# Kernel optimization log

Measured on AMD Instinct MI355X. Metric: run time of the kernel, lower is better.

The kernel has to match this reference:

```python
import jax, jax.numpy as jnp
import numpy as np

PI = np.pi


def setup_inputs() -> dict:
    key = jax.random.key(0)
    ks = jax.random.split(key, 20)
    B, L, D = 2, 1024, 512
    TP = 16      # n_sets(4) * planes_per_set(4)
    PP = 16      # pos_planes
    MAXL = 8192
    sc = 1.0 / np.sqrt(D)
    return {
        "x": jax.random.normal(ks[0], (B, L, D), jnp.float32),
        "Wk": jax.random.normal(ks[1], (TP, D), jnp.float32) * sc,
        "bk": jnp.zeros((TP,), jnp.float32),
        "Wq": jax.random.normal(ks[2], (TP, D), jnp.float32) * sc,
        "bq": jnp.zeros((TP,), jnp.float32),
        "Wv": jax.random.normal(ks[3], (D, D), jnp.float32) * sc,
        "bv": jnp.zeros((D,), jnp.float32),
        "ln_g": jnp.ones((D,), jnp.float32),
        "ln_b": jnp.zeros((D,), jnp.float32),
        "Wo": jax.random.normal(ks[4], (D, D), jnp.float32) * sc,
        "bo": jnp.zeros((D,), jnp.float32),
        "set_w": jnp.ones((4,), jnp.float32),
        "pos_phases": jax.random.normal(ks[5], (MAXL, PP), jnp.float32) * PI,
        "pos_weight": jnp.ones((1,), jnp.float32),
        "Wg1": jax.random.normal(ks[6], (D // 2, D), jnp.float32) * sc,
        "bg1": jnp.zeros((D // 2,), jnp.float32),
        "Wg2": jax.random.normal(ks[7], (1, D // 2), jnp.float32) * np.sqrt(2.0 / D),
        "bg2": jnp.zeros((1,), jnp.float32),
    }


def reference(x, Wk, bk, Wq, bq, Wv, bv, ln_g, ln_b, Wo, bo,
              set_w, pos_phases, pos_weight, Wg1, bg1, Wg2, bg2):
    B, L, D = x.shape
    n_sets, pps = 4, 4

    # --- content phasor memory ---
    kp = jnp.tanh(x @ Wk.T + bk) * PI                       # [B,L,16]
    qp = jnp.tanh(x @ Wq.T + bq) * PI
    key_ph = jnp.exp(1j * kp).reshape(B, L, n_sets, pps)    # [B,L,S,P] c64
    qry_ph = jnp.exp(1j * qp).reshape(B, L, n_sets, pps)
    Vr = x @ Wv.T + bv                                       # [B,L,D]
    V = Vr.astype(jnp.complex64)

    bound = key_ph[..., None] * V[:, :, None, None, :]       # [B,L,S,P,D] c64
    mem = jnp.cumsum(bound, axis=1)                          # prefix-sum memory
    retr = (mem * jnp.conj(qry_ph)[..., None]).sum(axis=3).real   # [B,L,S,D]
    w = jax.nn.softmax(set_w)
    content = (retr * w[None, None, :, None]).sum(axis=2)    # [B,L,D]

    # --- positional cos/sin memory ---
    ph = pos_phases[:L]                                      # [L,PP]
    c = jnp.cos(ph)[None]                                    # [1,L,PP]
    s = jnp.sin(ph)[None]
    br = Vr[:, :, None, :] * c[..., None]                    # [B,L,PP,D]
    bi = Vr[:, :, None, :] * s[..., None]
    mr = jnp.cumsum(br, axis=1)
    mi = jnp.cumsum(bi, axis=1)
    pos = (mr * c[..., None] + mi * s[..., None]).sum(axis=2)  # [B,L,D]

    # --- gate, mix, normalize, output proj ---
    g = jax.nn.sigmoid(
        jax.nn.gelu(x @ Wg1.T + bg1, approximate=False) @ Wg2.T + bg2)  # [B,L,1]
    total = g * content + (1.0 - g) * jax.nn.sigmoid(pos_weight) * pos
    norm = jnp.sqrt(jnp.arange(1, L + 1, dtype=x.dtype) * pps)[None, :, None]
    t = total / norm
    mu = t.mean(-1, keepdims=True)
    var = ((t - mu) ** 2).mean(-1, keepdims=True)
    tn = (t - mu) / jnp.sqrt(var + 1e-5) * ln_g + ln_b
    return x + tn @ Wo.T + bo
```

## Files before the change

kernel.cpp:

```cpp
#include <hip/hip_runtime.h>
#include <math.h>

#define PI_F 3.14159265358979323846f
#define BB 2
#define LL 1024
#define DD 512
#define NCH 64
#define CHUNK 32
#define NCHUNK (LL/CHUNK)
#define YN 896
#define NW 1408

typedef __attribute__((ext_vector_type(8))) short short8;
typedef __attribute__((ext_vector_type(4))) float floatx4;
typedef const __attribute__((address_space(1))) unsigned int cgu32;
typedef __attribute__((address_space(3))) unsigned int lu32;

__device__ __forceinline__ unsigned short f2bf(float f){
    unsigned u = __float_as_uint(f);
    unsigned r = (u + 0x7fff + ((u >> 16) & 1)) >> 16;
    return (unsigned short)r;
}

__global__ __launch_bounds__(128) void k_prep(
    const float* __restrict__ Wv, const float* __restrict__ Wg1,
    const float* __restrict__ Wk, const float* __restrict__ Wq,
    const float* __restrict__ Wo,
    const float* __restrict__ bv, const float* __restrict__ bg1,
    const float* __restrict__ bk, const float* __restrict__ bq,
    const float* __restrict__ bo,
    unsigned short* __restrict__ Wb, float* __restrict__ bcat)
{
    const int n = blockIdx.x, tid = threadIdx.x;
    const float* src = (n<512) ? Wv  + (size_t)n*512
                     : (n<768) ? Wg1 + (size_t)(n-512)*512
                     : (n<784) ? Wk  + (size_t)(n-768)*512
                     : (n<800) ? Wq  + (size_t)(n-784)*512
                     : (n<896) ? (const float*)0
                               : Wo  + (size_t)(n-896)*512;
    float4 v = make_float4(0.f,0.f,0.f,0.f);
    if (src) v = ((const float4*)src)[tid];
    ushort4 o; o.x=f2bf(v.x); o.y=f2bf(v.y); o.z=f2bf(v.z); o.w=f2bf(v.w);
    ((ushort4*)(Wb + (size_t)n*512))[tid] = o;
    if (tid == 0)
        bcat[n] = (n<512)?bv[n] : (n<768)?bg1[n-512] : (n<784)?bk[n-768]
                : (n<800)?bq[n-784] : (n<896)?0.f : bo[n-896];
}

__global__ __launch_bounds__(256) void k_xb(
    const float* __restrict__ x, unsigned short* __restrict__ xb)
{
    const int i = blockIdx.x*256 + threadIdx.x;
    float4 v = ((const float4*)x)[i];
    ushort4 o; o.x=f2bf(v.x); o.y=f2bf(v.y); o.z=f2bf(v.z); o.w=f2bf(v.w);
    ((ushort4*)xb)[i] = o;
}

__device__ __forceinline__ void gemm64x64(
    const unsigned short* Ag, const unsigned short* Bg,
    short* As, short* Bs, int tid, floatx4 acc[2][2])
{
    const int lane = tid & 63, w = tid >> 6;
    const int wm = w & 1, wn = w >> 1;
    const int q = lane >> 4, m15 = lane & 15;
    for (int kt = 0; kt < 512; kt += 64) {
        __syncthreads();
        #pragma unroll
        for (int i = 0; i < 2; ++i) {
            const int rowbase = (w*2 + i) * 8;
            const int r  = rowbase + (lane >> 3);
            const int gb = (lane & 7) ^ (r & 7);
            const unsigned short* ga = Ag + (size_t)r*512 + kt + gb*8;
            const unsigned short* gbp = Bg + (size_t)r*512 + kt + gb*8;
            __builtin_amdgcn_global_load_lds((cgu32*)(const void*)ga,
                                             (lu32*)(As + rowbase*64), 16, 0, 0);
            __builtin_amdgcn_global_load_lds((cgu32*)(const void*)gbp,
                                             (lu32*)(Bs + rowbase*64), 16, 0, 0);
        }
        __syncthreads();
        #pragma unroll
        for (int k32 = 0; k32 < 64; k32 += 32) {
            short8 af[2], bf[2];
            #pragma unroll
            for (int t = 0; t < 2; ++t) {
                const int ra  = 32*wm + 16*t + m15;
                const int sba = ((k32>>3) + q) ^ (ra & 7);
                af[t] = *(const short8*)(As + ra*64 + sba*8);
                const int rb  = 32*wn + 16*t + m15;
                const int sbb = ((k32>>3) + q) ^ (rb & 7);
                bf[t] = *(const short8*)(Bs + rb*64 + sbb*8);
            }
            #pragma unroll
            for (int mt = 0; mt < 2; ++mt)
                #pragma unroll
                for (int nt = 0; nt < 2; ++nt)
                    acc[mt][nt] = __builtin_amdgcn_mfma_f32_16x16x32_bf16(
                        af[mt], bf[nt], acc[mt][nt], 0, 0, 0);
        }
    }
}

__global__ __launch_bounds__(256) void kg1(
    const unsigned short* __restrict__ xb, const unsigned short* __restrict__ Wb,
    const float* __restrict__ bcat, float* __restrict__ Y)
{
    __shared__ short As[64*64], Bs[64*64];
    const int tid = threadIdx.x;
    const int row0 = blockIdx.x*64, n0 = blockIdx.y*64;
    floatx4 acc[2][2];
    #pragma unroll
    for (int mt=0;mt<2;++mt)
        #pragma unroll
        for (int nt=0;nt<2;++nt) acc[mt][nt] = (floatx4){0.f,0.f,0.f,0.f};
    gemm64x64(xb + (size_t)row0*512, Wb + (size_t)n0*512, As, Bs, tid, acc);
    const int lane = tid & 63, w = tid >> 6;
    const int wm = w & 1, wn = w >> 1, q = lane >> 4, m15 = lane & 15;
    #pragma unroll
    for (int mt=0;mt<2;++mt)
        #pragma unroll
        for (int nt=0;nt<2;++nt){
            const int n = n0 + 32*wn + 16*nt + m15;
            const float b = bcat[n];
            #pragma unroll
            for (int reg=0;reg<4;++reg){
                const int m = row0 + 32*wm + 16*mt + q*4 + reg;
                Y[(size_t)m*YN + n] = acc[mt][nt][reg] + b;
            }
        }
}

__global__ __launch_bounds__(256) void k_act(
    const float* __restrict__ Y, const float* __restrict__ Wg2,
    const float* __restrict__ bg2, const float* __restrict__ set_w,
    const float* __restrict__ pos_phases, const float* __restrict__ pos_weight,
    float* __restrict__ aB, float* __restrict__ RB)
{
    const int tid = threadIdx.x, lane = tid & 63, w = tid >> 6;
    const int row0 = blockIdx.x * 8;
    float s0=set_w[0], s1=set_w[1], s2=set_w[2], s3=set_w[3];
    float m = fmaxf(fmaxf(s0,s1), fmaxf(s2,s3));
    float e0=expf(s0-m), e1=expf(s1-m), e2=expf(s2-m), e3=expf(s3-m);
    float esum = e0+e1+e2+e3;
    float spw = 1.f/(1.f+expf(-pos_weight[0]));
    float b2 = bg2[0];
    #pragma unroll
    for (int rr=0;rr<2;++rr){
        int row = row0 + w + 4*rr;
        const float* yrow = Y + (size_t)row*YN;
        float hs = 0.f;
        #pragma unroll
        for (int i=0;i<4;++i){
            float hv = yrow[512 + lane + 64*i];
            float ge = 0.5f*hv*(1.f + erff(hv*0.70710678118f));
            hs += ge * Wg2[lane + 64*i];
        }
        #pragma unroll
        for (int off=32; off; off>>=1) hs += __shfl_xor(hs, off, 64);
        float g = 1.f/(1.f+expf(-(hs + b2)));
        if (lane < 16){
            int j = lane;
            int l = row & (LL-1);
            float kang = PI_F*tanhf(yrow[768 + j]);
            float qang = PI_F*tanhf(yrow[784 + j]);
            float wsm = (j<4?e0: j<8?e1: j<12?e2: e3) / esum;
            float rnorm = 1.f/(2.f*sqrtf((float)(l+1)));
            float* arow = aB + (size_t)row*NCH;
            float* Rrow = RB + (size_t)row*NCH;
            arow[j]    = cosf(kang);
            arow[16+j] = sinf(kang);
            float cw = g*wsm*rnorm;
            Rrow[j]    = cw*cosf(qang);
            Rrow[16+j] = cw*sinf(qang);
            float ph = pos_phases[(size_t)l*16 + j];
            float pc = cosf(ph), ps = sinf(ph);
            arow[32+j] = pc; arow[48+j] = ps;
            float cp = (1.f-g)*spw*rnorm;
            Rrow[32+j] = cp*pc; Rrow[48+j] = cp*ps;
        }
    }
}

__global__ __launch_bounds__(128) void k2a_chunksum(
    const float* __restrict__ Y, const float* __restrict__ aB,
    float* __restrict__ P)
{
    const int c = blockIdx.x, b = blockIdx.y;
    const int d = blockIdx.z*128 + threadIdx.x;
    float S[NCH];
    #pragma unroll
    for (int k=0;k<NCH;++k) S[k]=0.f;
    for (int l=0;l<CHUNK;++l){
        const size_t rowi = (size_t)b*LL + (size_t)c*CHUNK + l;
        float v = Y[rowi*YN + d];
        const float* ar = aB + rowi*NCH;
        #pragma unroll
        for (int k=0;k<NCH;++k) S[k] = fmaf(ar[k], v, S[k]);
    }
    #pragma unroll
    for (int k=0;k<NCH;++k)
        P[(((size_t)b*NCHUNK + c)*NCH + k)*512 + d] = S[k];
}

__global__ __launch_bounds__(128) void k2b_prefix(float* __restrict__ P)
{
    const int k = blockIdx.x, b = blockIdx.y;
    const int d = blockIdx.z*128 + threadIdx.x;
    float run = 0.f;
    for (int c=0;c<NCHUNK;++c){
        size_t idx = (((size_t)b*NCHUNK + c)*NCH + k)*512 + d;
        float v = P[idx];
        P[idx] = run;
        run += v;
    }
}

__global__ __launch_bounds__(128) void k2c_scan(
    const float* __restrict__ Y, const float* __restrict__ aB,
    const float* __restrict__ RB, const float* __restrict__ P,
    float* __restrict__ T_)
{
    const int c = blockIdx.x, b = blockIdx.y;
    const int d = blockIdx.z*128 + threadIdx.x;
    float S[NCH];
    #pragma unroll
    for (int k=0;k<NCH;++k)
        S[k] = P[(((size_t)b*NCHUNK + c)*NCH + k)*512 + d];
    for (int l=0;l<CHUNK;++l){
        const size_t rowi = (size_t)b*LL + (size_t)c*CHUNK + l;
        float v = Y[rowi*YN + d];
        const float* ar = aB + rowi*NCH;
        const float* rw = RB + rowi*NCH;
        float a0=0.f,a1=0.f,a2=0.f,a3=0.f;
        #pragma unroll
        for (int k=0;k<NCH;k+=4){
            S[k]   = fmaf(ar[k],   v, S[k]);   a0 = fmaf(rw[k],   S[k],   a0);
            S[k+1] = fmaf(ar[k+1], v, S[k+1]); a1 = fmaf(rw[k+1], S[k+1], a1);
            S[k+2] = fmaf(ar[k+2], v, S[k+2]); a2 = fmaf(rw[k+2], S[k+2], a2);
            S[k+3] = fmaf(ar[k+3], v, S[k+3]); a3 = fmaf(rw[k+3], S[k+3], a3);
        }
        T_[rowi*512 + d] = (a0+a1)+(a2+a3);
    }
}

__global__ __launch_bounds__(256) void k_ln(
    const float* __restrict__ T_, const float* __restrict__ ln_g,
    const float* __restrict__ ln_b, unsigned short* __restrict__ Tn)
{
    const int tid = threadIdx.x, lane = tid & 63;
    const int r = blockIdx.x*4 + (tid >> 6);
    const float4* tr = (const float4*)(T_ + (size_t)r*512);
    float4 v0 = tr[lane], v1 = tr[lane+64];
    float s  = v0.x+v0.y+v0.z+v0.w + v1.x+v1.y+v1.z+v1.w;
    float sq = v0.x*v0.x+v0.y*v0.y+v0.z*v0.z+v0.w*v0.w
             + v1.x*v1.x+v1.y*v1.y+v1.z*v1.z+v1.w*v1.w;
    #pragma unroll
    for (int off=32; off; off>>=1){ s += __shfl_xor(s, off, 64); sq += __shfl_xor(sq, off, 64); }
    float mu  = s*(1.f/512.f);
    float var = sq*(1.f/512.f) - mu*mu;
    float rsd = rsqrtf(var + 1e-5f);
    const float4* g4 = (const float4*)ln_g;
    const float4* b4 = (const float4*)ln_b;
    float4 g0 = g4[lane], g1 = g4[lane+64], bb0 = b4[lane], bb1 = b4[lane+64];
    ushort4 o0, o1;
    o0.x = f2bf((v0.x-mu)*rsd*g0.x + bb0.x);
    o0.y = f2bf((v0.y-mu)*rsd*g0.y + bb0.y);
    o0.z = f2bf((v0.z-mu)*rsd*g0.z + bb0.z);
    o0.w = f2bf((v0.w-mu)*rsd*g0.w + bb0.w);
    o1.x = f2bf((v1.x-mu)*rsd*g1.x + bb1.x);
    o1.y = f2bf((v1.y-mu)*rsd*g1.y + bb1.y);
    o1.z = f2bf((v1.z-mu)*rsd*g1.z + bb1.z);
    o1.w = f2bf((v1.w-mu)*rsd*g1.w + bb1.w);
    ushort4* dst = (ushort4*)(Tn + (size_t)r*512);
    dst[lane] = o0; dst[lane+64] = o1;
}

__global__ __launch_bounds__(256) void kg2(
    const unsigned short* __restrict__ Tn, const unsigned short* __restrict__ Wb,
    const float* __restrict__ bcat, const float* __restrict__ x,
    float* __restrict__ out)
{
    __shared__ short As[64*64], Bs[64*64];
    const int tid = threadIdx.x;
    const int row0 = blockIdx.x*64, n0 = blockIdx.y*64;
    floatx4 acc[2][2];
    #pragma unroll
    for (int mt=0;mt<2;++mt)
        #pragma unroll
        for (int nt=0;nt<2;++nt) acc[mt][nt] = (floatx4){0.f,0.f,0.f,0.f};
    gemm64x64(Tn + (size_t)row0*512, Wb + (size_t)(896+n0)*512, As, Bs, tid, acc);
    const int lane = tid & 63, w = tid >> 6;
    const int wm = w & 1, wn = w >> 1, q = lane >> 4, m15 = lane & 15;
    #pragma unroll
    for (int mt=0;mt<2;++mt)
        #pragma unroll
        for (int nt=0;nt<2;++nt){
            const int n = n0 + 32*wn + 16*nt + m15;
            const float b = bcat[896 + n];
            #pragma unroll
            for (int reg=0;reg<4;++reg){
                const int m = row0 + 32*wm + 16*mt + q*4 + reg;
                out[(size_t)m*512 + n] = x[(size_t)m*512 + n] + acc[mt][nt][reg] + b;
            }
        }
}

extern "C" void kernel_launch(void* const* d_in, const int* in_sizes, int n_in,
                              void* d_out, int out_size, void* d_ws, size_t ws_size,
                              hipStream_t stream) {
    const float* x    = (const float*)d_in[0];
    const float* Wk   = (const float*)d_in[1];
    const float* bk   = (const float*)d_in[2];
    const float* Wq   = (const float*)d_in[3];
    const float* bq   = (const float*)d_in[4];
    const float* Wv   = (const float*)d_in[5];
    const float* bv   = (const float*)d_in[6];
    const float* ln_g = (const float*)d_in[7];
    const float* ln_b = (const float*)d_in[8];
    const float* Wo   = (const float*)d_in[9];
    const float* bo   = (const float*)d_in[10];
    const float* set_w      = (const float*)d_in[11];
    const float* pos_phases = (const float*)d_in[12];
    const float* pos_weight = (const float*)d_in[13];
    const float* Wg1  = (const float*)d_in[14];
    const float* bg1  = (const float*)d_in[15];
    const float* Wg2  = (const float*)d_in[16];
    const float* bg2  = (const float*)d_in[17];
    float* out = (float*)d_out;

    float* ws   = (float*)d_ws;
    float* Y    = ws;
    float* P    = Y  + (size_t)2048*YN;
    float* T_   = P  + (size_t)BB*NCHUNK*NCH*512;
    float* aB   = T_ + (size_t)2048*512;
    float* RB   = aB + (size_t)2048*NCH;
    float* bcat = RB + (size_t)2048*NCH;
    unsigned short* Wb = (unsigned short*)(bcat + NW);
    unsigned short* xb = Wb + (size_t)NW*512;
    unsigned short* Tn = xb + (size_t)2048*512;

    k_prep<<<dim3(NW), 128, 0, stream>>>(Wv,Wg1,Wk,Wq,Wo, bv,bg1,bk,bq,bo, Wb, bcat);
    k_xb<<<dim3(2048*512/(256*4)), 256, 0, stream>>>(x, xb);
    kg1<<<dim3(2048/64, YN/64), 256, 0, stream>>>(xb, Wb, bcat, Y);
    k_act<<<dim3(BB*LL/8), 256, 0, stream>>>(Y, Wg2, bg2, set_w, pos_phases, pos_weight, aB, RB);
    k2a_chunksum<<<dim3(NCHUNK, BB, 4), 128, 0, stream>>>(Y, aB, P);
    k2b_prefix<<<dim3(NCH, BB, 4), 128, 0, stream>>>(P);
    k2c_scan<<<dim3(NCHUNK, BB, 4), 128, 0, stream>>>(Y, aB, RB, P, T_);
    k_ln<<<dim3(2048/4), 256, 0, stream>>>(T_, ln_g, ln_b, Tn);
    kg2<<<dim3(2048/64, 512/64), 256, 0, stream>>>(Tn, Wb, bcat, x, out);
}
```

Baseline: 167.1 us.

## Recast chunked phasor scan as bf16 MFMA matmuls and fuse layernorm

Replaces the scalar FMA chunk-sum and intra-chunk scan with bf16 MFMA matmuls. The value projection is stored transposed in bf16, the chunk-local causal mixing becomes a masked R·a^T matrix, and chunk prefix states go to bf16. LayerNorm is fused into the scan kernel, and the x-to-bf16 conversion is merged into the weight prep kernel, removing two launches and the fp32 intermediates. The bf16 storage of the scan state and the coefficients lowers precision, and the scan kernel's shared-memory footprint grows.

```diff
diff --git a/kernel.cpp b/kernel.cpp
--- a/kernel.cpp
+++ b/kernel.cpp
@@ -4,12 +4,11 @@
 #define PI_F 3.14159265358979323846f
 #define BB 2
 #define LL 1024
-#define DD 512
 #define NCH 64
 #define CHUNK 32
 #define NCHUNK (LL/CHUNK)
-#define YN 896
 #define NW 1408
+#define YH 384
 
 typedef __attribute__((ext_vector_type(8))) short short8;
 typedef __attribute__((ext_vector_type(4))) float floatx4;
@@ -28,32 +27,32 @@
     const float* __restrict__ Wo,
     const float* __restrict__ bv, const float* __restrict__ bg1,
     const float* __restrict__ bk, const float* __restrict__ bq,
-    const float* __restrict__ bo,
-    unsigned short* __restrict__ Wb, float* __restrict__ bcat)
-{
-    const int n = blockIdx.x, tid = threadIdx.x;
-    const float* src = (n<512) ? Wv  + (size_t)n*512
-                     : (n<768) ? Wg1 + (size_t)(n-512)*512
-                     : (n<784) ? Wk  + (size_t)(n-768)*512
-                     : (n<800) ? Wq  + (size_t)(n-784)*512
-                     : (n<896) ? (const float*)0
-                               : Wo  + (size_t)(n-896)*512;
-    float4 v = make_float4(0.f,0.f,0.f,0.f);
-    if (src) v = ((const float4*)src)[tid];
-    ushort4 o; o.x=f2bf(v.x); o.y=f2bf(v.y); o.z=f2bf(v.z); o.w=f2bf(v.w);
-    ((ushort4*)(Wb + (size_t)n*512))[tid] = o;
-    if (tid == 0)
-        bcat[n] = (n<512)?bv[n] : (n<768)?bg1[n-512] : (n<784)?bk[n-768]
-                : (n<800)?bq[n-784] : (n<896)?0.f : bo[n-896];
-}
-
-__global__ __launch_bounds__(256) void k_xb(
-    const float* __restrict__ x, unsigned short* __restrict__ xb)
-{
-    const int i = blockIdx.x*256 + threadIdx.x;
-    float4 v = ((const float4*)x)[i];
-    ushort4 o; o.x=f2bf(v.x); o.y=f2bf(v.y); o.z=f2bf(v.z); o.w=f2bf(v.w);
-    ((ushort4*)xb)[i] = o;
+    const float* __restrict__ bo, const float* __restrict__ x,
+    unsigned short* __restrict__ Wb, float* __restrict__ bcat,
+    unsigned short* __restrict__ xb)
+{
+    const int bid = blockIdx.x, tid = threadIdx.x;
+    if (bid < NW){
+        const int n = bid;
+        const float* src = (n<512) ? Wv  + (size_t)n*512
+                         : (n<768) ? Wg1 + (size_t)(n-512)*512
+                         : (n<784) ? Wk  + (size_t)(n-768)*512
+                         : (n<800) ? Wq  + (size_t)(n-784)*512
+                         : (n<896) ? (const float*)0
+                                   : Wo  + (size_t)(n-896)*512;
+        float4 v = make_float4(0.f,0.f,0.f,0.f);
+        if (src) v = ((const float4*)src)[tid];
+        ushort4 o; o.x=f2bf(v.x); o.y=f2bf(v.y); o.z=f2bf(v.z); o.w=f2bf(v.w);
+        ((ushort4*)(Wb + (size_t)n*512))[tid] = o;
+        if (tid == 0)
+            bcat[n] = (n<512)?bv[n] : (n<768)?bg1[n-512] : (n<784)?bk[n-768]
+                    : (n<800)?bq[n-784] : (n<896)?0.f : bo[n-896];
+    } else {
+        const size_t i = (size_t)(bid - NW)*128 + tid;
+        float4 v = ((const float4*)x)[i];
+        ushort4 o; o.x=f2bf(v.x); o.y=f2bf(v.y); o.z=f2bf(v.z); o.w=f2bf(v.w);
+        ((ushort4*)xb)[i] = o;
+    }
 }
 
 __device__ __forceinline__ void gemm64x64(
@@ -70,7 +69,7 @@
             const int rowbase = (w*2 + i) * 8;
             const int r  = rowbase + (lane >> 3);
             const int gb = (lane & 7) ^ (r & 7);
-            const unsigned short* ga = Ag + (size_t)r*512 + kt + gb*8;
+            const unsigned short* ga  = Ag + (size_t)r*512 + kt + gb*8;
             const unsigned short* gbp = Bg + (size_t)r*512 + kt + gb*8;
             __builtin_amdgcn_global_load_lds((cgu32*)(const void*)ga,
                                              (lu32*)(As + rowbase*64), 16, 0, 0);
@@ -102,7 +101,8 @@
 
 __global__ __launch_bounds__(256) void kg1(
     const unsigned short* __restrict__ xb, const unsigned short* __restrict__ Wb,
-    const float* __restrict__ bcat, float* __restrict__ Y)
+    const float* __restrict__ bcat, unsigned short* __restrict__ Vt,
+    float* __restrict__ Yh)
 {
     __shared__ short As[64*64], Bs[64*64];
     const int tid = threadIdx.x;
@@ -115,25 +115,44 @@
     gemm64x64(xb + (size_t)row0*512, Wb + (size_t)n0*512, As, Bs, tid, acc);
     const int lane = tid & 63, w = tid >> 6;
     const int wm = w & 1, wn = w >> 1, q = lane >> 4, m15 = lane & 15;
-    #pragma unroll
-    for (int mt=0;mt<2;++mt)
-        #pragma unroll
-        for (int nt=0;nt<2;++nt){
-            const int n = n0 + 32*wn + 16*nt + m15;
-            const float b = bcat[n];
-            #pragma unroll
-            for (int reg=0;reg<4;++reg){
-                const int m = row0 + 32*wm + 16*mt + q*4 + reg;
-                Y[(size_t)m*YN + n] = acc[mt][nt][reg] + b;
-            }
-        }
+    if (n0 < 512){
+        const int b = row0 >> 10, lb = row0 & 1023;
+        #pragma unroll
+        for (int mt=0;mt<2;++mt)
+            #pragma unroll
+            for (int nt=0;nt<2;++nt){
+                const int d = n0 + 32*wn + 16*nt + m15;
+                const float bb = bcat[d];
+                const int l0 = lb + 32*wm + 16*mt + q*4;
+                ushort4 o;
+                o.x = f2bf(acc[mt][nt][0] + bb);
+                o.y = f2bf(acc[mt][nt][1] + bb);
+                o.z = f2bf(acc[mt][nt][2] + bb);
+                o.w = f2bf(acc[mt][nt][3] + bb);
+                *(ushort4*)(Vt + ((size_t)(b*512 + d))*1024 + l0) = o;
+            }
+    } else {
+        #pragma unroll
+        for (int mt=0;mt<2;++mt)
+            #pragma unroll
+            for (int nt=0;nt<2;++nt){
+                const int n = n0 + 32*wn + 16*nt + m15;
+                const float bb = bcat[n];
+                #pragma unroll
+                for (int reg=0;reg<4;++reg){
+                    const int m = row0 + 32*wm + 16*mt + q*4 + reg;
+                    Yh[(size_t)m*YH + (n-512)] = acc[mt][nt][reg] + bb;
+                }
+            }
+    }
 }
 
 __global__ __launch_bounds__(256) void k_act(
-    const float* __restrict__ Y, const float* __restrict__ Wg2,
+    const float* __restrict__ Yh, const float* __restrict__ Wg2,
     const float* __restrict__ bg2, const float* __restrict__ set_w,
     const float* __restrict__ pos_phases, const float* __restrict__ pos_weight,
-    float* __restrict__ aB, float* __restrict__ RB)
+    unsigned short* __restrict__ ab, unsigned short* __restrict__ Rb,
+    unsigned short* __restrict__ aT)
 {
     const int tid = threadIdx.x, lane = tid & 63, w = tid >> 6;
     const int row0 = blockIdx.x * 8;
@@ -146,11 +165,11 @@
     #pragma unroll
     for (int rr=0;rr<2;++rr){
         int row = row0 + w + 4*rr;
-        const float* yrow = Y + (size_t)row*YN;
+        const float* yrow = Yh + (size_t)row*YH;
         float hs = 0.f;
         #pragma unroll
         for (int i=0;i<4;++i){
-            float hv = yrow[512 + lane + 64*i];
+            float hv = yrow[lane + 64*i];
             float ge = 0.5f*hv*(1.f + erff(hv*0.70710678118f));
             hs += ge * Wg2[lane + 64*i];
         }
@@ -160,118 +179,193 @@
         if (lane < 16){
             int j = lane;
             int l = row & (LL-1);
-            float kang = PI_F*tanhf(yrow[768 + j]);
-            float qang = PI_F*tanhf(yrow[784 + j]);
+            int b = row >> 10;
+            float kang = PI_F*tanhf(yrow[256 + j]);
+            float qang = PI_F*tanhf(yrow[272 + j]);
             float wsm = (j<4?e0: j<8?e1: j<12?e2: e3) / esum;
             float rnorm = 1.f/(2.f*sqrtf((float)(l+1)));
-            float* arow = aB + (size_t)row*NCH;
-            float* Rrow = RB + (size_t)row*NCH;
-            arow[j]    = cosf(kang);
-            arow[16+j] = sinf(kang);
+            float av[4], rv[4];
+            av[0] = cosf(kang); av[1] = sinf(kang);
             float cw = g*wsm*rnorm;
-            Rrow[j]    = cw*cosf(qang);
-            Rrow[16+j] = cw*sinf(qang);
+            rv[0] = cw*cosf(qang); rv[1] = cw*sinf(qang);
             float ph = pos_phases[(size_t)l*16 + j];
             float pc = cosf(ph), ps = sinf(ph);
-            arow[32+j] = pc; arow[48+j] = ps;
+            av[2] = pc; av[3] = ps;
             float cp = (1.f-g)*spw*rnorm;
-            Rrow[32+j] = cp*pc; Rrow[48+j] = cp*ps;
-        }
-    }
-}
-
-__global__ __launch_bounds__(128) void k2a_chunksum(
-    const float* __restrict__ Y, const float* __restrict__ aB,
+            rv[2] = cp*pc; rv[3] = cp*ps;
+            unsigned short* arow = ab + (size_t)row*NCH;
+            unsigned short* Rrow = Rb + (size_t)row*NCH;
+            #pragma unroll
+            for (int t=0;t<4;++t){
+                arow[16*t + j] = f2bf(av[t]);
+                Rrow[16*t + j] = f2bf(rv[t]);
+                aT[((size_t)b*NCH + 16*t + j)*1024 + l] = f2bf(av[t]);
+            }
+        }
+    }
+}
+
+__global__ __launch_bounds__(256) void k2a_chunksum(
+    const unsigned short* __restrict__ aT, const unsigned short* __restrict__ Vt,
     float* __restrict__ P)
 {
-    const int c = blockIdx.x, b = blockIdx.y;
-    const int d = blockIdx.z*128 + threadIdx.x;
-    float S[NCH];
-    #pragma unroll
-    for (int k=0;k<NCH;++k) S[k]=0.f;
-    for (int l=0;l<CHUNK;++l){
-        const size_t rowi = (size_t)b*LL + (size_t)c*CHUNK + l;
-        float v = Y[rowi*YN + d];
-        const float* ar = aB + rowi*NCH;
-        #pragma unroll
-        for (int k=0;k<NCH;++k) S[k] = fmaf(ar[k], v, S[k]);
-    }
-    #pragma unroll
-    for (int k=0;k<NCH;++k)
-        P[(((size_t)b*NCHUNK + c)*NCH + k)*512 + d] = S[k];
-}
-
-__global__ __launch_bounds__(128) void k2b_prefix(float* __restrict__ P)
-{
-    const int k = blockIdx.x, b = blockIdx.y;
-    const int d = blockIdx.z*128 + threadIdx.x;
+    const int c = blockIdx.x, b = blockIdx.y, z = blockIdx.z;
+    const int tid = threadIdx.x, lane = tid & 63, w = tid >> 6;
+    const int q = lane >> 4, m15 = lane & 15;
+    short8 af[4];
+    #pragma unroll
+    for (int mt=0;mt<4;++mt)
+        af[mt] = *(const short8*)(aT + ((size_t)b*NCH + 16*mt + m15)*1024 + c*32 + q*8);
+    floatx4 acc[4][4];
+    #pragma unroll
+    for (int mt=0;mt<4;++mt)
+        #pragma unroll
+        for (int nt=0;nt<4;++nt) acc[mt][nt] = (floatx4){0.f,0.f,0.f,0.f};
+    #pragma unroll
+    for (int nt=0;nt<4;++nt){
+        const int d = z*256 + w*64 + 16*nt + m15;
+        short8 bf = *(const short8*)(Vt + ((size_t)(b*512 + d))*1024 + c*32 + q*8);
+        #pragma unroll
+        for (int mt=0;mt<4;++mt)
+            acc[mt][nt] = __builtin_amdgcn_mfma_f32_16x16x32_bf16(af[mt], bf, acc[mt][nt], 0,0,0);
+    }
+    float* Pc = P + ((size_t)(b*NCHUNK + c))*512*NCH;
+    #pragma unroll
+    for (int mt=0;mt<4;++mt)
+        #pragma unroll
+        for (int nt=0;nt<4;++nt){
+            const int d = z*256 + w*64 + 16*nt + m15;
+            const int ch0 = 16*mt + q*4;
+            *(floatx4*)(Pc + (size_t)d*NCH + ch0) = acc[mt][nt];
+        }
+}
+
+__global__ __launch_bounds__(256) void k2b_prefix(
+    const float* __restrict__ P, unsigned short* __restrict__ S0t)
+{
+    const int b = blockIdx.y;
+    const size_t idx = (size_t)blockIdx.x*256 + threadIdx.x;
     float run = 0.f;
     for (int c=0;c<NCHUNK;++c){
-        size_t idx = (((size_t)b*NCHUNK + c)*NCH + k)*512 + d;
-        float v = P[idx];
-        P[idx] = run;
+        const size_t o = ((size_t)(b*NCHUNK + c))*512*NCH + idx;
+        float v = P[o];
+        S0t[o] = f2bf(run);
         run += v;
     }
 }
 
-__global__ __launch_bounds__(128) void k2c_scan(
-    const float* __restrict__ Y, const float* __restrict__ aB,
-    const float* __restrict__ RB, const float* __restrict__ P,
-    float* __restrict__ T_)
-{
+__global__ __launch_bounds__(256) void k2c_scan(
+    const unsigned short* __restrict__ ab, const unsigned short* __restrict__ Rb,
+    const unsigned short* __restrict__ Vt, const unsigned short* __restrict__ S0t,
+    const float* __restrict__ ln_g, const float* __restrict__ ln_b,
+    unsigned short* __restrict__ Tn)
+{
+    __shared__ short Msh[32*32];
+    __shared__ float Tsh[32*512];
     const int c = blockIdx.x, b = blockIdx.y;
-    const int d = blockIdx.z*128 + threadIdx.x;
-    float S[NCH];
-    #pragma unroll
-    for (int k=0;k<NCH;++k)
-        S[k] = P[(((size_t)b*NCHUNK + c)*NCH + k)*512 + d];
-    for (int l=0;l<CHUNK;++l){
-        const size_t rowi = (size_t)b*LL + (size_t)c*CHUNK + l;
-        float v = Y[rowi*YN + d];
-        const float* ar = aB + rowi*NCH;
-        const float* rw = RB + rowi*NCH;
-        float a0=0.f,a1=0.f,a2=0.f,a3=0.f;
-        #pragma unroll
-        for (int k=0;k<NCH;k+=4){
-            S[k]   = fmaf(ar[k],   v, S[k]);   a0 = fmaf(rw[k],   S[k],   a0);
-            S[k+1] = fmaf(ar[k+1], v, S[k+1]); a1 = fmaf(rw[k+1], S[k+1], a1);
-            S[k+2] = fmaf(ar[k+2], v, S[k+2]); a2 = fmaf(rw[k+2], S[k+2], a2);
-            S[k+3] = fmaf(ar[k+3], v, S[k+3]); a3 = fmaf(rw[k+3], S[k+3], a3);
-        }
-        T_[rowi*512 + d] = (a0+a1)+(a2+a3);
-    }
-}
-
-__global__ __launch_bounds__(256) void k_ln(
-    const float* __restrict__ T_, const float* __restrict__ ln_g,
-    const float* __restrict__ ln_b, unsigned short* __restrict__ Tn)
-{
-    const int tid = threadIdx.x, lane = tid & 63;
-    const int r = blockIdx.x*4 + (tid >> 6);
-    const float4* tr = (const float4*)(T_ + (size_t)r*512);
-    float4 v0 = tr[lane], v1 = tr[lane+64];
-    float s  = v0.x+v0.y+v0.z+v0.w + v1.x+v1.y+v1.z+v1.w;
-    float sq = v0.x*v0.x+v0.y*v0.y+v0.z*v0.z+v0.w*v0.w
-             + v1.x*v1.x+v1.y*v1.y+v1.z*v1.z+v1.w*v1.w;
-    #pragma unroll
-    for (int off=32; off; off>>=1){ s += __shfl_xor(s, off, 64); sq += __shfl_xor(sq, off, 64); }
-    float mu  = s*(1.f/512.f);
-    float var = sq*(1.f/512.f) - mu*mu;
-    float rsd = rsqrtf(var + 1e-5f);
-    const float4* g4 = (const float4*)ln_g;
-    const float4* b4 = (const float4*)ln_b;
-    float4 g0 = g4[lane], g1 = g4[lane+64], bb0 = b4[lane], bb1 = b4[lane+64];
-    ushort4 o0, o1;
-    o0.x = f2bf((v0.x-mu)*rsd*g0.x + bb0.x);
-    o0.y = f2bf((v0.y-mu)*rsd*g0.y + bb0.y);
-    o0.z = f2bf((v0.z-mu)*rsd*g0.z + bb0.z);
-    o0.w = f2bf((v0.w-mu)*rsd*g0.w + bb0.w);
-    o1.x = f2bf((v1.x-mu)*rsd*g1.x + bb1.x);
-    o1.y = f2bf((v1.y-mu)*rsd*g1.y + bb1.y);
-    o1.z = f2bf((v1.z-mu)*rsd*g1.z + bb1.z);
-    o1.w = f2bf((v1.w-mu)*rsd*g1.w + bb1.w);
-    ushort4* dst = (ushort4*)(Tn + (size_t)r*512);
-    dst[lane] = o0; dst[lane+64] = o1;
+    const int tid = threadIdx.x, lane = tid & 63, w = tid >> 6;
+    const int q = lane >> 4, m15 = lane & 15;
+    const int grow = b*1024 + c*32;
+
+    if (w == 0){
+        floatx4 mcc[2][2];
+        #pragma unroll
+        for (int mt=0;mt<2;++mt)
+            #pragma unroll
+            for (int nt=0;nt<2;++nt) mcc[mt][nt] = (floatx4){0.f,0.f,0.f,0.f};
+        #pragma unroll
+        for (int ks=0;ks<2;++ks){
+            short8 ra[2], bb[2];
+            #pragma unroll
+            for (int t=0;t<2;++t){
+                ra[t] = *(const short8*)(Rb + (size_t)(grow + 16*t + m15)*NCH + ks*32 + q*8);
+                bb[t] = *(const short8*)(ab + (size_t)(grow + 16*t + m15)*NCH + ks*32 + q*8);
+            }
+            #pragma unroll
+            for (int mt=0;mt<2;++mt)
+                #pragma unroll
+                for (int nt=0;nt<2;++nt)
+                    mcc[mt][nt] = __builtin_amdgcn_mfma_f32_16x16x32_bf16(
+                        ra[mt], bb[nt], mcc[mt][nt], 0,0,0);
+        }
+        #pragma unroll
+        for (int mt=0;mt<2;++mt)
+            #pragma unroll
+            for (int nt=0;nt<2;++nt){
+                const int nl = 16*nt + m15;
+                #pragma unroll
+                for (int reg=0;reg<4;++reg){
+                    const int ml = 16*mt + q*4 + reg;
+                    Msh[ml*32 + nl] = (nl <= ml) ? (short)f2bf(mcc[mt][nt][reg]) : (short)0;
+                }
+            }
+    }
+    __syncthreads();
+
+    short8 a1[2], a2[2][2];
+    #pragma unroll
+    for (int mt=0;mt<2;++mt){
+        a1[mt] = *(const short8*)(Msh + (16*mt + m15)*32 + q*8);
+        #pragma unroll
+        for (int ks=0;ks<2;++ks)
+            a2[ks][mt] = *(const short8*)(Rb + (size_t)(grow + 16*mt + m15)*NCH + ks*32 + q*8);
+    }
+    floatx4 acc[2][8];
+    #pragma unroll
+    for (int mt=0;mt<2;++mt)
+        #pragma unroll
+        for (int nt=0;nt<8;++nt) acc[mt][nt] = (floatx4){0.f,0.f,0.f,0.f};
+    const unsigned short* S0c = S0t + ((size_t)(b*NCHUNK + c))*512*NCH;
+    #pragma unroll
+    for (int nt=0;nt<8;++nt){
+        const int d = w*128 + 16*nt + m15;
+        short8 b1 = *(const short8*)(Vt + ((size_t)(b*512 + d))*1024 + c*32 + q*8);
+        #pragma unroll
+        for (int mt=0;mt<2;++mt)
+            acc[mt][nt] = __builtin_amdgcn_mfma_f32_16x16x32_bf16(a1[mt], b1, acc[mt][nt], 0,0,0);
+        #pragma unroll
+        for (int ks=0;ks<2;++ks){
+            short8 b2 = *(const short8*)(S0c + (size_t)d*NCH + ks*32 + q*8);
+            #pragma unroll
+            for (int mt=0;mt<2;++mt)
+                acc[mt][nt] = __builtin_amdgcn_mfma_f32_16x16x32_bf16(a2[ks][mt], b2, acc[mt][nt], 0,0,0);
+        }
+    }
+    #pragma unroll
+    for (int mt=0;mt<2;++mt)
+        #pragma unroll
+        for (int nt=0;nt<8;++nt){
+            const int d = w*128 + 16*nt + m15;
+            #pragma unroll
+            for (int reg=0;reg<4;++reg)
+                Tsh[(16*mt + q*4 + reg)*512 + d] = acc[mt][nt][reg];
+        }
+    __syncthreads();
+
+    #pragma unroll
+    for (int i=0;i<8;++i){
+        const int r = w*8 + i;
+        float s=0.f, sq=0.f;
+        #pragma unroll
+        for (int t=0;t<8;++t){
+            float v = Tsh[r*512 + lane + 64*t];
+            s += v; sq += v*v;
+        }
+        #pragma unroll
+        for (int off=32; off; off>>=1){
+            s += __shfl_xor(s, off, 64); sq += __shfl_xor(sq, off, 64);
+        }
+        float mu  = s*(1.f/512.f);
+        float var = sq*(1.f/512.f) - mu*mu;
+        float rsd = rsqrtf(var + 1e-5f);
+        unsigned short* trow = Tn + (size_t)(grow + r)*512;
+        #pragma unroll
+        for (int t=0;t<8;++t){
+            const int d = lane + 64*t;
+            float v = (Tsh[r*512 + d] - mu)*rsd*ln_g[d] + ln_b[d];
+            trow[d] = f2bf(v);
+        }
+    }
 }
 
 __global__ __launch_bounds__(256) void kg2(
@@ -295,11 +389,11 @@
         #pragma unroll
         for (int nt=0;nt<2;++nt){
             const int n = n0 + 32*wn + 16*nt + m15;
-            const float b = bcat[896 + n];
+            const float bb = bcat[896 + n];
             #pragma unroll
             for (int reg=0;reg<4;++reg){
                 const int m = row0 + 32*wm + 16*mt + q*4 + reg;
-                out[(size_t)m*512 + n] = x[(size_t)m*512 + n] + acc[mt][nt][reg] + b;
+                out[(size_t)m*512 + n] = x[(size_t)m*512 + n] + acc[mt][nt][reg] + bb;
             }
         }
 }
@@ -328,23 +422,25 @@
     float* out = (float*)d_out;
 
     float* ws   = (float*)d_ws;
-    float* Y    = ws;
-    float* P    = Y  + (size_t)2048*YN;
-    float* T_   = P  + (size_t)BB*NCHUNK*NCH*512;
-    float* aB   = T_ + (size_t)2048*512;
-    float* RB   = aB + (size_t)2048*NCH;
-    float* bcat = RB + (size_t)2048*NCH;
-    unsigned short* Wb = (unsigned short*)(bcat + NW);
-    unsigned short* xb = Wb + (size_t)NW*512;
-    unsigned short* Tn = xb + (size_t)2048*512;
-
-    k_prep<<<dim3(NW), 128, 0, stream>>>(Wv,Wg1,Wk,Wq,Wo, bv,bg1,bk,bq,bo, Wb, bcat);
-    k_xb<<<dim3(2048*512/(256*4)), 256, 0, stream>>>(x, xb);
-    kg1<<<dim3(2048/64, YN/64), 256, 0, stream>>>(xb, Wb, bcat, Y);
-    k_act<<<dim3(BB*LL/8), 256, 0, stream>>>(Y, Wg2, bg2, set_w, pos_phases, pos_weight, aB, RB);
-    k2a_chunksum<<<dim3(NCHUNK, BB, 4), 128, 0, stream>>>(Y, aB, P);
-    k2b_prefix<<<dim3(NCH, BB, 4), 128, 0, stream>>>(P);
-    k2c_scan<<<dim3(NCHUNK, BB, 4), 128, 0, stream>>>(Y, aB, RB, P, T_);
-    k_ln<<<dim3(2048/4), 256, 0, stream>>>(T_, ln_g, ln_b, Tn);
+    float* Yh   = ws;
+    float* P    = Yh + (size_t)2048*YH;
+    float* bcat = P  + (size_t)BB*NCHUNK*512*NCH;
+    unsigned short* Wb  = (unsigned short*)(bcat + NW);
+    unsigned short* xb  = Wb  + (size_t)NW*512;
+    unsigned short* Vt  = xb  + (size_t)2048*512;
+    unsigned short* ab  = Vt  + (size_t)BB*512*1024;
+    unsigned short* Rb  = ab  + (size_t)2048*NCH;
+    unsigned short* aT  = Rb  + (size_t)2048*NCH;
+    unsigned short* S0t = aT  + (size_t)BB*NCH*1024;
+    unsigned short* Tn  = S0t + (size_t)BB*NCHUNK*512*NCH;
+
+    k_prep<<<dim3(NW + 2048), 128, 0, stream>>>(
+        Wv,Wg1,Wk,Wq,Wo, bv,bg1,bk,bq,bo, x, Wb, bcat, xb);
+    kg1<<<dim3(2048/64, 14), 256, 0, stream>>>(xb, Wb, bcat, Vt, Yh);
+    k_act<<<dim3(2048/8), 256, 0, stream>>>(
+        Yh, Wg2, bg2, set_w, pos_phases, pos_weight, ab, Rb, aT);
+    k2a_chunksum<<<dim3(NCHUNK, BB, 2), 256, 0, stream>>>(aT, Vt, P);
+    k2b_prefix<<<dim3(512*NCH/256, BB), 256, 0, stream>>>(P, S0t);
+    k2c_scan<<<dim3(NCHUNK, BB), 256, 0, stream>>>(ab, Rb, Vt, S0t, ln_g, ln_b, Tn);
     kg2<<<dim3(2048/64, 512/64), 256, 0, stream>>>(Tn, Wb, bcat, x, out);
 }
```

After: 134.5 us. 19.5% less time.
